# Kernel tuning notes

Measured on AMD Instinct MI355X. Metric: run time of the kernel, lower is better.

Reference implementation:

```python
import jax, jax.numpy as jnp
import numpy as np

B, L, D, H = 4, 2048, 512, 8
HD = D // H  # 64
MAX_REL = 4


def setup_inputs() -> dict:
    key = jax.random.key(0)
    ks = jax.random.split(key, 13)
    s = 1.0 / np.sqrt(D)
    return {
        "q": jax.random.normal(ks[0], (B, L, D), jnp.float32),
        "k": jax.random.normal(ks[1], (B, L, D), jnp.float32),
        "v": jax.random.normal(ks[2], (B, L, D), jnp.float32),
        "Wq": jax.random.normal(ks[3], (D, D), jnp.float32) * s,
        "bq": jax.random.normal(ks[4], (D,), jnp.float32) * 0.01,
        "Wk": jax.random.normal(ks[5], (D, D), jnp.float32) * s,
        "bk": jax.random.normal(ks[6], (D,), jnp.float32) * 0.01,
        "Wv": jax.random.normal(ks[7], (D, D), jnp.float32) * s,
        "bv": jax.random.normal(ks[8], (D,), jnp.float32) * 0.01,
        "Wo": jax.random.normal(ks[9], (D, D), jnp.float32) * s,
        "bo": jax.random.normal(ks[10], (D,), jnp.float32) * 0.01,
        "rel_k_table": jax.random.normal(ks[11], (2 * MAX_REL + 1, HD), jnp.float32),
        "rel_v_table": jax.random.normal(ks[12], (2 * MAX_REL + 1, HD), jnp.float32),
    }


def _to_heads(x):
    # [B, L, D] -> [B, H, L, HD]
    b, l, d = x.shape
    return x.reshape(b, l, H, d // H).transpose(0, 2, 1, 3)


def reference(q, k, v, Wq, bq, Wk, bk, Wv, bv, Wo, bo, rel_k_table, rel_v_table):
    # NOTE: in the source, the relative-attention output is overwritten by the
    # plain SDPA call immediately after, so observable math = SDPA only.
    # rel_k_table / rel_v_table are dead parameters (zero gradient).
    relu = jax.nn.relu
    qh = _to_heads(relu(q @ Wq.T + bq))  # [B,H,L,HD]
    kh = _to_heads(relu(k @ Wk.T + bk))
    vh = _to_heads(relu(v @ Wv.T + bv))
    # scale by sqrt(d_key)=sqrt(512), matching the original (not sqrt(head_dim))
    scores = jnp.einsum("bhqd,bhkd->bhqk", qh, kh) / jnp.sqrt(jnp.float32(D))
    attn = jax.nn.softmax(scores, axis=-1)
    out = jnp.einsum("bhqk,bhkd->bhqd", attn, vh)  # [B,H,L,HD]
    out = out.transpose(0, 2, 1, 3).reshape(B, L, D)
    return relu(out @ Wo.T + bo)
```

## Files before the change

### kernel.cpp

```cpp
#include <hip/hip_runtime.h>
#include <hip/hip_bf16.h>

#define B_  4
#define L_  2048
#define D_  512
#define H_  8
#define HD_ 64
#define M_  (B_ * L_)

typedef __bf16 bf16;
typedef __attribute__((ext_vector_type(8)))  __bf16 bf16x8;
typedef __attribute__((ext_vector_type(4)))  __bf16 bf16x4;
typedef __attribute__((ext_vector_type(16))) float  f32x16;

__device__ __forceinline__ f32x16 mfma32(bf16x8 a, bf16x8 b, f32x16 c) {
    return __builtin_amdgcn_mfma_f32_32x32x16_bf16(a, b, c, 0, 0, 0);
}

__device__ __forceinline__ void pack_body(const float* __restrict__ src,
                                          bf16* __restrict__ dst, int R,
                                          int m0, int k0)
{
    __shared__ __align__(16) bf16 tile[64][76];
    const int t = threadIdx.x;
#pragma unroll
    for (int rep = 0; rep < 4; rep++) {
        const int idx = rep * 256 + t;
        const int r = idx >> 4, c4 = idx & 15;
        const float4 f = *(const float4*)(src + (size_t)(m0 + r) * 512 + k0 + c4 * 4);
        bf16x4 v; v[0] = (bf16)f.x; v[1] = (bf16)f.y; v[2] = (bf16)f.z; v[3] = (bf16)f.w;
        *(bf16x4*)(&tile[r][c4 * 4]) = v;
    }
    __syncthreads();
#pragma unroll
    for (int rep = 0; rep < 2; rep++) {
        const int s = rep * 256 + t;
        const int ml = s & 63, kpl = s >> 6;
        const bf16x4 lo = *(const bf16x4*)(&tile[ml][kpl * 8]);
        const bf16x4 hi4 = *(const bf16x4*)(&tile[ml][kpl * 8 + 4]);
        bf16x8 v;
#pragma unroll
        for (int e = 0; e < 4; e++) { v[e] = lo[e]; v[e + 4] = hi4[e]; }
        *(bf16x8*)(dst + ((size_t)(k0 / 8 + kpl) * R + m0 + ml) * 8) = v;
    }
}

__global__ __launch_bounds__(256) void pack_all(
    const float* __restrict__ q, const float* __restrict__ k,
    const float* __restrict__ v,
    const float* __restrict__ W0, const float* __restrict__ W1,
    const float* __restrict__ W2, const float* __restrict__ W3,
    bf16* __restrict__ Wp, bf16* __restrict__ P0, bf16* __restrict__ P1,
    bf16* __restrict__ P2)
{
    const int z = blockIdx.z;
    if (z < 4) {
        if (blockIdx.x >= 8) return;
        const float* src = z == 0 ? W0 : z == 1 ? W1 : z == 2 ? W2 : W3;
        pack_body(src, Wp + (size_t)z * 64 * 512 * 8, 512, blockIdx.x * 64, blockIdx.y * 64);
    } else {
        const float* src = z == 4 ? q : z == 5 ? k : v;
        bf16* dst = z == 4 ? P0 : z == 5 ? P1 : P2;
        pack_body(src, dst, M_, blockIdx.x * 64, blockIdx.y * 64);
    }
}

struct PJob {
    const bf16* X; const bf16* W; const float* bias; void* out;
    float postmul; int mode;
};

__global__ __launch_bounds__(256, 3) void proj_kernel(PJob j0, PJob j1)
{
    const PJob jb = (blockIdx.z == 0) ? j0 : j1;
    const int w    = threadIdx.x >> 6;
    const int lane = threadIdx.x & 63;
    const int l31  = lane & 31;
    const int hi   = lane >> 5;
    const int m0 = blockIdx.x * 128;
    const int n0 = blockIdx.y * 64;
    const int mh = w & 1;
    const int nh = w >> 1;

    __shared__ __align__(16) bf16 Ab[2][16][64][8];
    __shared__ __align__(16) bf16 Bb[2][8][64][8];

    f32x16 acc[2];
#pragma unroll
    for (int mi = 0; mi < 2; mi++)
#pragma unroll
        for (int r = 0; r < 16; r++) acc[mi][r] = 0.0f;

    auto ldA = [&](int f, int k0) -> bf16x8 {
        return *(const bf16x8*)(jb.X + ((size_t)((k0 >> 3) + (f >> 2) * 2 + hi) * M_
                                        + m0 + (f & 3) * 32 + l31) * 8);
    };
    auto ldB = [&](int f, int k0) -> bf16x8 {
        return *(const bf16x8*)(jb.W + ((size_t)((k0 >> 3) + (f >> 1) * 2 + hi) * 512
                                        + n0 + (f & 1) * 32 + l31) * 8);
    };

    bf16x8 rA[3][4], rB[3][2];
#pragma unroll
    for (int i = 0; i < 4; i++) rA[0][i] = ldA(w * 4 + i, 0);
#pragma unroll
    for (int i = 0; i < 2; i++) rB[0][i] = ldB(w * 2 + i, 0);
#pragma unroll
    for (int i = 0; i < 4; i++) *(bf16x8*)(&Ab[0][w * 4 + i][lane][0]) = rA[0][i];
#pragma unroll
    for (int i = 0; i < 2; i++) *(bf16x8*)(&Bb[0][w * 2 + i][lane][0]) = rB[0][i];
#pragma unroll
    for (int s = 1; s < 3; s++) {
#pragma unroll
        for (int i = 0; i < 4; i++) rA[s][i] = ldA(w * 4 + i, s * 64);
#pragma unroll
        for (int i = 0; i < 2; i++) rB[s][i] = ldB(w * 2 + i, s * 64);
    }
    __syncthreads();

#pragma unroll
    for (int it = 0; it < 8; it++) {
        const int cur = it & 1;
        if (it < 5) {
            const int s = it % 3, kn = (it + 3) * 64;
#pragma unroll
            for (int i = 0; i < 4; i++) rA[s][i] = ldA(w * 4 + i, kn);
#pragma unroll
            for (int i = 0; i < 2; i++) rB[s][i] = ldB(w * 2 + i, kn);
        }
#pragma unroll
        for (int ks = 0; ks < 4; ks++) {
            const bf16x8 bfr = *(const bf16x8*)(&Bb[cur][ks * 2 + nh][lane][0]);
#pragma unroll
            for (int mi = 0; mi < 2; mi++) {
                const bf16x8 afr = *(const bf16x8*)(&Ab[cur][ks * 4 + mh * 2 + mi][lane][0]);
                acc[mi] = mfma32(afr, bfr, acc[mi]);
            }
        }
        if (it < 7) {
            const int s = (it + 1) % 3;
#pragma unroll
            for (int i = 0; i < 4; i++) *(bf16x8*)(&Ab[1 - cur][w * 4 + i][lane][0]) = rA[s][i];
#pragma unroll
            for (int i = 0; i < 2; i++) *(bf16x8*)(&Bb[1 - cur][w * 2 + i][lane][0]) = rB[s][i];
            __syncthreads();
        }
    }

    const int col = n0 + nh * 32 + l31;
    const float bn = jb.bias[col];
    const int mode = jb.mode;
#pragma unroll
    for (int mi = 0; mi < 2; mi++)
#pragma unroll
        for (int r = 0; r < 16; r++) {
            const int row = m0 + (mh * 2 + mi) * 32 + (r & 3) + 8 * (r >> 2) + 4 * hi;
            float v = fmaxf(acc[mi][r] + bn, 0.0f);
            if (mode == 2) {
                ((float*)jb.out)[(size_t)row * D_ + col] = v;
            } else {
                v *= jb.postmul;
                const int b = row >> 11, l = row & (L_ - 1);
                const int h = col >> 6,  hd = col & (HD_ - 1);
                const int bh = b * H_ + h;
                size_t idx;
                if (mode == 0) {
                    idx = ((size_t)bh * L_ + l) * HD_ + hd;
                } else if (mode == 1) {
                    idx = (((size_t)bh * 8 + (hd >> 3)) * L_ + l) * 8 + (hd & 7);
                } else {
                    const int swzl = (l & ~15) | (l & 3) | ((l & 4) << 1) | ((l & 8) >> 1);
                    idx = (((size_t)bh * 256 + (swzl >> 3)) * 64 + hd) * 8 + (swzl & 7);
                }
                ((bf16*)jb.out)[idx] = (bf16)v;
            }
        }
}

__global__ __launch_bounds__(128, 2) void attn_kernel(
    const bf16* __restrict__ qh, const bf16* __restrict__ Kp,
    const bf16* __restrict__ Vp, bf16* __restrict__ Op)
{
    const int w    = threadIdx.x >> 6;
    const int lane = threadIdx.x & 63;
    const int l31  = lane & 31;
    const int hi   = lane >> 5;
    const int bh   = blockIdx.y;
    const int qb   = blockIdx.x * 64 + w * 32;

    const bf16* Q   = qh + (size_t)bh * L_ * HD_;
    const bf16* Kpb = Kp + (size_t)bh * 8 * L_ * 8;
    const bf16* Vpb = Vp + (size_t)bh * 256 * 64 * 8;

    __shared__ __align__(16) bf16 Vb[2][8][64][8];

    bf16x8 qf[4];
#pragma unroll
    for (int ks = 0; ks < 4; ks++)
        qf[ks] = *(const bf16x8*)(Q + (size_t)(qb + l31) * HD_ + ks * 16 + hi * 8);

    f32x16 zz;
#pragma unroll
    for (int r = 0; r < 16; r++) zz[r] = 0.0f;
    f32x16 o0 = zz, o1 = zz, lacc = zz;
    bf16x8 ones;
#pragma unroll
    for (int u = 0; u < 8; u++) ones[u] = (bf16)1.0f;

    auto ldK = [&](int f, int t) -> bf16x8 {
        return *(const bf16x8*)(Kpb + ((size_t)((f >> 1) * 2 + hi) * L_
                                       + t * 64 + (f & 1) * 32 + l31) * 8);
    };
    auto ldV = [&](int f, int t) -> bf16x8 {
        return *(const bf16x8*)(Vpb + ((size_t)(t * 8 + (f >> 1) * 2 + hi) * 64
                                       + (f & 1) * 32 + l31) * 8);
    };

    bf16x8 kr[8], vr[2][4];
#pragma unroll
    for (int i = 0; i < 4; i++) vr[0][i] = ldV(w * 4 + i, 0);
#pragma unroll
    for (int i = 0; i < 4; i++) *(bf16x8*)(&Vb[0][w * 4 + i][lane][0]) = vr[0][i];
#pragma unroll
    for (int i = 0; i < 4; i++) vr[1][i] = ldV(w * 4 + i, 1);
#pragma unroll
    for (int i = 0; i < 4; i++) vr[0][i] = ldV(w * 4 + i, 2);
#pragma unroll
    for (int f = 0; f < 8; f++) kr[f] = ldK(f, 0);
    __syncthreads();

    auto tile_body = [&](int t, int cur, int nxt) {
        f32x16 s0 = mfma32(kr[0], qf[0], zz);
        f32x16 s1 = mfma32(kr[1], qf[0], zz);
#pragma unroll
        for (int ks = 1; ks < 4; ks++) {
            s0 = mfma32(kr[ks * 2 + 0], qf[ks], s0);
            s1 = mfma32(kr[ks * 2 + 1], qf[ks], s1);
        }
        if (t < 31) {
#pragma unroll
            for (int f = 0; f < 8; f++) kr[f] = ldK(f, t + 1);
        }

#pragma unroll
        for (int r = 0; r < 16; r++) s0[r] = __builtin_amdgcn_exp2f(s0[r]);
        {
            bf16x8 pf0, pf1;
#pragma unroll
            for (int u = 0; u < 8; u++) { pf0[u] = (bf16)s0[u]; pf1[u] = (bf16)s0[8 + u]; }
            o0   = mfma32(pf0, *(const bf16x8*)(&Vb[cur][0][lane][0]), o0);
            o1   = mfma32(pf0, *(const bf16x8*)(&Vb[cur][1][lane][0]), o1);
            lacc = mfma32(pf0, ones, lacc);
            o0   = mfma32(pf1, *(const bf16x8*)(&Vb[cur][2][lane][0]), o0);
            o1   = mfma32(pf1, *(const bf16x8*)(&Vb[cur][3][lane][0]), o1);
            lacc = mfma32(pf1, ones, lacc);
        }
#pragma unroll
        for (int r = 0; r < 16; r++) s1[r] = __builtin_amdgcn_exp2f(s1[r]);
        {
            bf16x8 pf2, pf3;
#pragma unroll
            for (int u = 0; u < 8; u++) { pf2[u] = (bf16)s1[u]; pf3[u] = (bf16)s1[8 + u]; }
            o0   = mfma32(pf2, *(const bf16x8*)(&Vb[cur][4][lane][0]), o0);
            o1   = mfma32(pf2, *(const bf16x8*)(&Vb[cur][5][lane][0]), o1);
            lacc = mfma32(pf2, ones, lacc);
            o0   = mfma32(pf3, *(const bf16x8*)(&Vb[cur][6][lane][0]), o0);
            o1   = mfma32(pf3, *(const bf16x8*)(&Vb[cur][7][lane][0]), o1);
            lacc = mfma32(pf3, ones, lacc);
        }

        if (t < 31) {
#pragma unroll
            for (int i = 0; i < 4; i++)
                *(bf16x8*)(&Vb[1 - cur][w * 4 + i][lane][0]) = vr[nxt][i];
            const int tn = (t + 3 < 32) ? t + 3 : 31;
#pragma unroll
            for (int i = 0; i < 4; i++) vr[nxt][i] = ldV(w * 4 + i, tn);
            __syncthreads();
        }
    };

    for (int tt = 0; tt < 16; tt++) {
        tile_body(2 * tt + 0, 0, 1);
        tile_body(2 * tt + 1, 1, 0);
    }

    const int b = bh >> 3, h = bh & 7;
#pragma unroll
    for (int r = 0; r < 16; r++) {
        const int rl = (r & 3) + 8 * (r >> 2) + 4 * hi;
        const float inv = 1.0f / lacc[r];
        const int m = b * L_ + qb + rl;
        const int c0 = h * HD_ + l31;
        Op[((size_t)(c0 >> 3) * M_ + m) * 8 + (c0 & 7)] = (bf16)(o0[r] * inv);
        const int c1 = c0 + 32;
        Op[((size_t)(c1 >> 3) * M_ + m) * 8 + (c1 & 7)] = (bf16)(o1[r] * inv);
    }
}

extern "C" void kernel_launch(void* const* d_in, const int* in_sizes, int n_in,
                              void* d_out, int out_size, void* d_ws, size_t ws_size,
                              hipStream_t stream)
{
    (void)in_sizes; (void)n_in; (void)out_size; (void)ws_size;
    const float* q  = (const float*)d_in[0];
    const float* k  = (const float*)d_in[1];
    const float* v  = (const float*)d_in[2];
    const float* Wq = (const float*)d_in[3];
    const float* bq = (const float*)d_in[4];
    const float* Wk = (const float*)d_in[5];
    const float* bk = (const float*)d_in[6];
    const float* Wv = (const float*)d_in[7];
    const float* bv = (const float*)d_in[8];
    const float* Wo = (const float*)d_in[9];
    const float* bo = (const float*)d_in[10];
    float* out = (float*)d_out;

    char* ws = (char*)d_ws;
    const size_t MB = 1024 * 1024;
    bf16* P0  = (bf16*)(ws);
    bf16* P1  = (bf16*)(ws + 8 * MB);
    bf16* P2  = (bf16*)(ws + 16 * MB);
    bf16* Wp  = (bf16*)(ws + 24 * MB);
    bf16* qh  = (bf16*)(d_out);
    bf16* Kp  = (bf16*)((char*)d_out + 8 * MB);
    bf16* Vp  = P0;
    bf16* Opb = P1;

    bf16* Wqp = Wp;
    bf16* Wkp = Wp + (size_t)64 * 512 * 8;
    bf16* Wvp = Wp + (size_t)2 * 64 * 512 * 8;
    bf16* Wop = Wp + (size_t)3 * 64 * 512 * 8;

    const float SCALE_LOG2E = 0.06377946282349575f;

    dim3 pb(256);
    pack_all<<<dim3(128, 8, 7), pb, 0, stream>>>(q, k, v, Wq, Wk, Wv, Wo,
                                                 Wp, P0, P1, P2);

    PJob jq{P0, Wqp, bq, qh, SCALE_LOG2E, 0};
    PJob jk{P1, Wkp, bk, Kp, 1.0f, 1};
    proj_kernel<<<dim3(64, 8, 2), pb, 0, stream>>>(jq, jk);

    PJob jv{P2, Wvp, bv, Vp, 1.0f, 3};
    proj_kernel<<<dim3(64, 8, 1), pb, 0, stream>>>(jv, jv);

    attn_kernel<<<dim3(32, 32), dim3(128), 0, stream>>>(qh, Kp, Vp, Opb);

    PJob jo{Opb, Wop, bo, out, 1.0f, 2};
    proj_kernel<<<dim3(64, 8, 1), pb, 0, stream>>>(jo, jo);
}
```

Before: 197.6 us.

## Use single-wave attention blocks with register V, XCD-aware mapping, fused QKV projection

The attention kernel moves from 2-wave blocks that share V through double-buffered LDS and barriers to 1-wave blocks that load V fragments straight into registers, so LDS and __syncthreads go away. Blocks are remapped so all query tiles of a given (batch, head) land on the same XCD, improving L2 reuse of K/V, and s_setprio is raised around the MFMA bursts. When the workspace is large enough, V gets its own buffer so the Q, K and V projections can run as one 3-way launch instead of two. The cost is more register pressure and duplicate global V loads per wave, relying on L2 hits to absorb them.

```diff
diff --git a/kernel.cpp b/kernel.cpp
--- a/kernel.cpp
+++ b/kernel.cpp
@@ -70,9 +70,9 @@
     float postmul; int mode;
 };
 
-__global__ __launch_bounds__(256, 3) void proj_kernel(PJob j0, PJob j1)
-{
-    const PJob jb = (blockIdx.z == 0) ? j0 : j1;
+__global__ __launch_bounds__(256, 3) void proj_kernel(PJob j0, PJob j1, PJob j2)
+{
+    const PJob jb = (blockIdx.z == 0) ? j0 : (blockIdx.z == 1) ? j1 : j2;
     const int w    = threadIdx.x >> 6;
     const int lane = threadIdx.x & 63;
     const int l31  = lane & 31;
@@ -177,22 +177,23 @@
         }
 }
 
-__global__ __launch_bounds__(128, 2) void attn_kernel(
+__global__ __launch_bounds__(64, 2) void attn_kernel(
     const bf16* __restrict__ qh, const bf16* __restrict__ Kp,
     const bf16* __restrict__ Vp, bf16* __restrict__ Op)
 {
-    const int w    = threadIdx.x >> 6;
-    const int lane = threadIdx.x & 63;
+    const int lane = threadIdx.x;
     const int l31  = lane & 31;
     const int hi   = lane >> 5;
-    const int bh   = blockIdx.y;
-    const int qb   = blockIdx.x * 64 + w * 32;
+
+    const int lin  = blockIdx.x + (blockIdx.y << 6);
+    const int xcd  = lin & 7;
+    const int slot = lin >> 3;
+    const int bh   = (xcd << 2) + (slot >> 6);
+    const int qb   = (slot & 63) << 5;
 
     const bf16* Q   = qh + (size_t)bh * L_ * HD_;
     const bf16* Kpb = Kp + (size_t)bh * 8 * L_ * 8;
     const bf16* Vpb = Vp + (size_t)bh * 256 * 64 * 8;
-
-    __shared__ __align__(16) bf16 Vb[2][8][64][8];
 
     bf16x8 qf[4];
 #pragma unroll
@@ -216,20 +217,15 @@
                                        + (f & 1) * 32 + l31) * 8);
     };
 
-    bf16x8 kr[8], vr[2][4];
-#pragma unroll
-    for (int i = 0; i < 4; i++) vr[0][i] = ldV(w * 4 + i, 0);
-#pragma unroll
-    for (int i = 0; i < 4; i++) *(bf16x8*)(&Vb[0][w * 4 + i][lane][0]) = vr[0][i];
-#pragma unroll
-    for (int i = 0; i < 4; i++) vr[1][i] = ldV(w * 4 + i, 1);
-#pragma unroll
-    for (int i = 0; i < 4; i++) vr[0][i] = ldV(w * 4 + i, 2);
+    bf16x8 kr[8], vf[8];
 #pragma unroll
     for (int f = 0; f < 8; f++) kr[f] = ldK(f, 0);
-    __syncthreads();
-
-    auto tile_body = [&](int t, int cur, int nxt) {
+#pragma unroll
+    for (int f = 0; f < 8; f++) vf[f] = ldV(f, 0);
+
+#pragma unroll 2
+    for (int t = 0; t < 32; t++) {
+        __builtin_amdgcn_s_setprio(1);
         f32x16 s0 = mfma32(kr[0], qf[0], zz);
         f32x16 s1 = mfma32(kr[1], qf[0], zz);
 #pragma unroll
@@ -237,6 +233,7 @@
             s0 = mfma32(kr[ks * 2 + 0], qf[ks], s0);
             s1 = mfma32(kr[ks * 2 + 1], qf[ks], s1);
         }
+        __builtin_amdgcn_s_setprio(0);
         if (t < 31) {
 #pragma unroll
             for (int f = 0; f < 8; f++) kr[f] = ldK(f, t + 1);
@@ -244,45 +241,39 @@
 
 #pragma unroll
         for (int r = 0; r < 16; r++) s0[r] = __builtin_amdgcn_exp2f(s0[r]);
-        {
-            bf16x8 pf0, pf1;
-#pragma unroll
-            for (int u = 0; u < 8; u++) { pf0[u] = (bf16)s0[u]; pf1[u] = (bf16)s0[8 + u]; }
-            o0   = mfma32(pf0, *(const bf16x8*)(&Vb[cur][0][lane][0]), o0);
-            o1   = mfma32(pf0, *(const bf16x8*)(&Vb[cur][1][lane][0]), o1);
-            lacc = mfma32(pf0, ones, lacc);
-            o0   = mfma32(pf1, *(const bf16x8*)(&Vb[cur][2][lane][0]), o0);
-            o1   = mfma32(pf1, *(const bf16x8*)(&Vb[cur][3][lane][0]), o1);
-            lacc = mfma32(pf1, ones, lacc);
-        }
+        bf16x8 pf0, pf1;
+#pragma unroll
+        for (int u = 0; u < 8; u++) { pf0[u] = (bf16)s0[u]; pf1[u] = (bf16)s0[8 + u]; }
+        __builtin_amdgcn_s_setprio(1);
+        o0   = mfma32(pf0, vf[0], o0);
+        o1   = mfma32(pf0, vf[1], o1);
+        lacc = mfma32(pf0, ones, lacc);
+        o0   = mfma32(pf1, vf[2], o0);
+        o1   = mfma32(pf1, vf[3], o1);
+        lacc = mfma32(pf1, ones, lacc);
+        __builtin_amdgcn_s_setprio(0);
+        if (t < 31) {
+#pragma unroll
+            for (int f = 0; f < 4; f++) vf[f] = ldV(f, t + 1);
+        }
+
 #pragma unroll
         for (int r = 0; r < 16; r++) s1[r] = __builtin_amdgcn_exp2f(s1[r]);
-        {
-            bf16x8 pf2, pf3;
-#pragma unroll
-            for (int u = 0; u < 8; u++) { pf2[u] = (bf16)s1[u]; pf3[u] = (bf16)s1[8 + u]; }
-            o0   = mfma32(pf2, *(const bf16x8*)(&Vb[cur][4][lane][0]), o0);
-            o1   = mfma32(pf2, *(const bf16x8*)(&Vb[cur][5][lane][0]), o1);
-            lacc = mfma32(pf2, ones, lacc);
-            o0   = mfma32(pf3, *(const bf16x8*)(&Vb[cur][6][lane][0]), o0);
-            o1   = mfma32(pf3, *(const bf16x8*)(&Vb[cur][7][lane][0]), o1);
-            lacc = mfma32(pf3, ones, lacc);
-        }
-
+        bf16x8 pf2, pf3;
+#pragma unroll
+        for (int u = 0; u < 8; u++) { pf2[u] = (bf16)s1[u]; pf3[u] = (bf16)s1[8 + u]; }
+        __builtin_amdgcn_s_setprio(1);
+        o0   = mfma32(pf2, vf[4], o0);
+        o1   = mfma32(pf2, vf[5], o1);
+        lacc = mfma32(pf2, ones, lacc);
+        o0   = mfma32(pf3, vf[6], o0);
+        o1   = mfma32(pf3, vf[7], o1);
+        lacc = mfma32(pf3, ones, lacc);
+        __builtin_amdgcn_s_setprio(0);
         if (t < 31) {
 #pragma unroll
-            for (int i = 0; i < 4; i++)
-                *(bf16x8*)(&Vb[1 - cur][w * 4 + i][lane][0]) = vr[nxt][i];
-            const int tn = (t + 3 < 32) ? t + 3 : 31;
-#pragma unroll
-            for (int i = 0; i < 4; i++) vr[nxt][i] = ldV(w * 4 + i, tn);
-            __syncthreads();
-        }
-    };
-
-    for (int tt = 0; tt < 16; tt++) {
-        tile_body(2 * tt + 0, 0, 1);
-        tile_body(2 * tt + 1, 1, 0);
+            for (int f = 4; f < 8; f++) vf[f] = ldV(f, t + 1);
+        }
     }
 
     const int b = bh >> 3, h = bh & 7;
@@ -302,7 +293,7 @@
                               void* d_out, int out_size, void* d_ws, size_t ws_size,
                               hipStream_t stream)
 {
-    (void)in_sizes; (void)n_in; (void)out_size; (void)ws_size;
+    (void)in_sizes; (void)n_in; (void)out_size;
     const float* q  = (const float*)d_in[0];
     const float* k  = (const float*)d_in[1];
     const float* v  = (const float*)d_in[2];
@@ -324,7 +315,6 @@
     bf16* Wp  = (bf16*)(ws + 24 * MB);
     bf16* qh  = (bf16*)(d_out);
     bf16* Kp  = (bf16*)((char*)d_out + 8 * MB);
-    bf16* Vp  = P0;
     bf16* Opb = P1;
 
     bf16* Wqp = Wp;
@@ -338,15 +328,26 @@
     pack_all<<<dim3(128, 8, 7), pb, 0, stream>>>(q, k, v, Wq, Wk, Wv, Wo,
                                                  Wp, P0, P1, P2);
 
-    PJob jq{P0, Wqp, bq, qh, SCALE_LOG2E, 0};
-    PJob jk{P1, Wkp, bk, Kp, 1.0f, 1};
-    proj_kernel<<<dim3(64, 8, 2), pb, 0, stream>>>(jq, jk);
-
-    PJob jv{P2, Wvp, bv, Vp, 1.0f, 3};
-    proj_kernel<<<dim3(64, 8, 1), pb, 0, stream>>>(jv, jv);
-
-    attn_kernel<<<dim3(32, 32), dim3(128), 0, stream>>>(qh, Kp, Vp, Opb);
+    if (ws_size >= (size_t)34 * MB) {
+        bf16* VpN = (bf16*)(ws + 26 * MB);
+        PJob jq{P0, Wqp, bq, qh,  SCALE_LOG2E, 0};
+        PJob jk{P1, Wkp, bk, Kp,  1.0f, 1};
+        PJob jv{P2, Wvp, bv, VpN, 1.0f, 3};
+        proj_kernel<<<dim3(64, 8, 3), pb, 0, stream>>>(jq, jk, jv);
+
+        attn_kernel<<<dim3(64, 32), dim3(64), 0, stream>>>(qh, Kp, VpN, Opb);
+    } else {
+        bf16* Vp = P0;
+        PJob jq{P0, Wqp, bq, qh, SCALE_LOG2E, 0};
+        PJob jk{P1, Wkp, bk, Kp, 1.0f, 1};
+        proj_kernel<<<dim3(64, 8, 2), pb, 0, stream>>>(jq, jk, jk);
+
+        PJob jv{P2, Wvp, bv, Vp, 1.0f, 3};
+        proj_kernel<<<dim3(64, 8, 1), pb, 0, stream>>>(jv, jv, jv);
+
+        attn_kernel<<<dim3(64, 32), dim3(64), 0, stream>>>(qh, Kp, Vp, Opb);
+    }
 
     PJob jo{Opb, Wop, bo, out, 1.0f, 2};
-    proj_kernel<<<dim3(64, 8, 1), pb, 0, stream>>>(jo, jo);
-}
+    proj_kernel<<<dim3(64, 8, 1), pb, 0, stream>>>(jo, jo, jo);
+}
```

After: 202.5 us. 2.5% more time.

## Fuse fp32-to-bf16 activation conversion into QKV projection and remap attention blocks per XCD

Applied to the files above, without the earlier changes.

The separate pack pass that converted q/k/v activations to bf16 is removed. The QKV projection now loads fp32 rows directly, converts them in registers before staging to shared memory, and runs Q, K and V in a single launch. Attention blocks are remapped so that each XCD handles a contiguous set of batch-heads, which is meant to improve L2 reuse of K/V. The cost is doubled global read bytes for A tiles and extra conversion work inside the GEMM loop, along with the register pressure that comes with it.

```diff
diff --git a/kernel.cpp b/kernel.cpp
--- a/kernel.cpp
+++ b/kernel.cpp
@@ -45,34 +45,24 @@
     }
 }
 
-__global__ __launch_bounds__(256) void pack_all(
-    const float* __restrict__ q, const float* __restrict__ k,
-    const float* __restrict__ v,
+__global__ __launch_bounds__(256) void pack_w(
     const float* __restrict__ W0, const float* __restrict__ W1,
     const float* __restrict__ W2, const float* __restrict__ W3,
-    bf16* __restrict__ Wp, bf16* __restrict__ P0, bf16* __restrict__ P1,
-    bf16* __restrict__ P2)
+    bf16* __restrict__ Wp)
 {
     const int z = blockIdx.z;
-    if (z < 4) {
-        if (blockIdx.x >= 8) return;
-        const float* src = z == 0 ? W0 : z == 1 ? W1 : z == 2 ? W2 : W3;
-        pack_body(src, Wp + (size_t)z * 64 * 512 * 8, 512, blockIdx.x * 64, blockIdx.y * 64);
-    } else {
-        const float* src = z == 4 ? q : z == 5 ? k : v;
-        bf16* dst = z == 4 ? P0 : z == 5 ? P1 : P2;
-        pack_body(src, dst, M_, blockIdx.x * 64, blockIdx.y * 64);
-    }
+    const float* src = z == 0 ? W0 : z == 1 ? W1 : z == 2 ? W2 : W3;
+    pack_body(src, Wp + (size_t)z * 64 * 512 * 8, 512, blockIdx.x * 64, blockIdx.y * 64);
 }
 
 struct PJob {
-    const bf16* X; const bf16* W; const float* bias; void* out;
-    float postmul; int mode;
+    const bf16* X; const float* Xf; const bf16* W; const float* bias;
+    void* out; float postmul; int mode;
 };
 
-__global__ __launch_bounds__(256, 3) void proj_kernel(PJob j0, PJob j1)
-{
-    const PJob jb = (blockIdx.z == 0) ? j0 : j1;
+template<bool FP32A>
+__device__ __forceinline__ void proj_body(const PJob jb)
+{
     const int w    = threadIdx.x >> 6;
     const int lane = threadIdx.x & 63;
     const int l31  = lane & 31;
@@ -95,38 +85,80 @@
         return *(const bf16x8*)(jb.X + ((size_t)((k0 >> 3) + (f >> 2) * 2 + hi) * M_
                                         + m0 + (f & 3) * 32 + l31) * 8);
     };
+    auto ldAf = [&](int f, int k0, float4* d) {
+        const int row  = m0 + (f & 3) * 32 + l31;
+        const int koct = (k0 >> 3) + (f >> 2) * 2 + hi;
+        const float* p = jb.Xf + (size_t)row * 512 + koct * 8;
+        d[0] = *(const float4*)p;
+        d[1] = *(const float4*)(p + 4);
+    };
+    auto cv8 = [](const float4* d) -> bf16x8 {
+        bf16x8 v;
+        v[0] = (bf16)d[0].x; v[1] = (bf16)d[0].y;
+        v[2] = (bf16)d[0].z; v[3] = (bf16)d[0].w;
+        v[4] = (bf16)d[1].x; v[5] = (bf16)d[1].y;
+        v[6] = (bf16)d[1].z; v[7] = (bf16)d[1].w;
+        return v;
+    };
     auto ldB = [&](int f, int k0) -> bf16x8 {
         return *(const bf16x8*)(jb.W + ((size_t)((k0 >> 3) + (f >> 1) * 2 + hi) * 512
                                         + n0 + (f & 1) * 32 + l31) * 8);
     };
 
-    bf16x8 rA[3][4], rB[3][2];
-#pragma unroll
-    for (int i = 0; i < 4; i++) rA[0][i] = ldA(w * 4 + i, 0);
+    bf16x8 rA[3][4];
+    float4 rAf[2][4][2];
+    bf16x8 rB[3][2];
+
+    if constexpr (FP32A) {
+#pragma unroll
+        for (int i = 0; i < 4; i++) ldAf(w * 4 + i, 0, rAf[0][i]);
+#pragma unroll
+        for (int i = 0; i < 4; i++)
+            *(bf16x8*)(&Ab[0][w * 4 + i][lane][0]) = cv8(rAf[0][i]);
+#pragma unroll
+        for (int i = 0; i < 4; i++) ldAf(w * 4 + i, 64, rAf[1][i]);
+    } else {
+#pragma unroll
+        for (int i = 0; i < 4; i++) rA[0][i] = ldA(w * 4 + i, 0);
+#pragma unroll
+        for (int i = 0; i < 4; i++)
+            *(bf16x8*)(&Ab[0][w * 4 + i][lane][0]) = rA[0][i];
+#pragma unroll
+        for (int s = 1; s < 3; s++)
+#pragma unroll
+            for (int i = 0; i < 4; i++) rA[s][i] = ldA(w * 4 + i, s * 64);
+    }
 #pragma unroll
     for (int i = 0; i < 2; i++) rB[0][i] = ldB(w * 2 + i, 0);
 #pragma unroll
-    for (int i = 0; i < 4; i++) *(bf16x8*)(&Ab[0][w * 4 + i][lane][0]) = rA[0][i];
-#pragma unroll
-    for (int i = 0; i < 2; i++) *(bf16x8*)(&Bb[0][w * 2 + i][lane][0]) = rB[0][i];
-#pragma unroll
-    for (int s = 1; s < 3; s++) {
-#pragma unroll
-        for (int i = 0; i < 4; i++) rA[s][i] = ldA(w * 4 + i, s * 64);
+    for (int i = 0; i < 2; i++)
+        *(bf16x8*)(&Bb[0][w * 2 + i][lane][0]) = rB[0][i];
+#pragma unroll
+    for (int s = 1; s < 3; s++)
 #pragma unroll
         for (int i = 0; i < 2; i++) rB[s][i] = ldB(w * 2 + i, s * 64);
-    }
     __syncthreads();
 
 #pragma unroll
     for (int it = 0; it < 8; it++) {
         const int cur = it & 1;
+        if constexpr (FP32A) {
+            if (it < 6) {
+#pragma unroll
+                for (int i = 0; i < 4; i++)
+                    ldAf(w * 4 + i, (it + 2) * 64, rAf[it & 1][i]);
+            }
+        } else {
+            if (it < 5) {
+#pragma unroll
+                for (int i = 0; i < 4; i++)
+                    rA[it % 3][i] = ldA(w * 4 + i, (it + 3) * 64);
+            }
+        }
         if (it < 5) {
-            const int s = it % 3, kn = (it + 3) * 64;
-#pragma unroll
-            for (int i = 0; i < 4; i++) rA[s][i] = ldA(w * 4 + i, kn);
-#pragma unroll
-            for (int i = 0; i < 2; i++) rB[s][i] = ldB(w * 2 + i, kn);
+#pragma unroll
+            for (int i = 0; i < 2; i++)
+                rB[it % 3][i] = ldB(w * 2 + i, (it + 3) * 64);
         }
 #pragma unroll
         for (int ks = 0; ks < 4; ks++) {
@@ -138,11 +170,18 @@
             }
         }
         if (it < 7) {
-            const int s = (it + 1) % 3;
-#pragma unroll
-            for (int i = 0; i < 4; i++) *(bf16x8*)(&Ab[1 - cur][w * 4 + i][lane][0]) = rA[s][i];
-#pragma unroll
-            for (int i = 0; i < 2; i++) *(bf16x8*)(&Bb[1 - cur][w * 2 + i][lane][0]) = rB[s][i];
+            if constexpr (FP32A) {
+#pragma unroll
+                for (int i = 0; i < 4; i++)
+                    *(bf16x8*)(&Ab[1 - cur][w * 4 + i][lane][0]) = cv8(rAf[(it + 1) & 1][i]);
+            } else {
+#pragma unroll
+                for (int i = 0; i < 4; i++)
+                    *(bf16x8*)(&Ab[1 - cur][w * 4 + i][lane][0]) = rA[(it + 1) % 3][i];
+            }
+#pragma unroll
+            for (int i = 0; i < 2; i++)
+                *(bf16x8*)(&Bb[1 - cur][w * 2 + i][lane][0]) = rB[(it + 1) % 3][i];
             __syncthreads();
         }
     }
@@ -177,6 +216,18 @@
         }
 }
 
+__global__ __launch_bounds__(256, 3) void proj_kernel(PJob j0, PJob j1, PJob j2)
+{
+    const PJob jb = (blockIdx.z == 0) ? j0 : (blockIdx.z == 1) ? j1 : j2;
+    proj_body<false>(jb);
+}
+
+__global__ __launch_bounds__(256, 3) void proj_qkv_kernel(PJob j0, PJob j1, PJob j2)
+{
+    const PJob jb = (blockIdx.z == 0) ? j0 : (blockIdx.z == 1) ? j1 : j2;
+    proj_body<true>(jb);
+}
+
 __global__ __launch_bounds__(128, 2) void attn_kernel(
     const bf16* __restrict__ qh, const bf16* __restrict__ Kp,
     const bf16* __restrict__ Vp, bf16* __restrict__ Op)
@@ -185,8 +236,12 @@
     const int lane = threadIdx.x & 63;
     const int l31  = lane & 31;
     const int hi   = lane >> 5;
-    const int bh   = blockIdx.y;
-    const int qb   = blockIdx.x * 64 + w * 32;
+
+    const int lin  = blockIdx.x + (blockIdx.y << 5);
+    const int xcd  = lin & 7;
+    const int slot = lin >> 3;
+    const int bh   = (xcd << 2) + (slot >> 5);
+    const int qb   = (slot & 31) * 64 + w * 32;
 
     const bf16* Q   = qh + (size_t)bh * L_ * HD_;
     const bf16* Kpb = Kp + (size_t)bh * 8 * L_ * 8;
@@ -318,14 +373,11 @@
 
     char* ws = (char*)d_ws;
     const size_t MB = 1024 * 1024;
-    bf16* P0  = (bf16*)(ws);
-    bf16* P1  = (bf16*)(ws + 8 * MB);
-    bf16* P2  = (bf16*)(ws + 16 * MB);
-    bf16* Wp  = (bf16*)(ws + 24 * MB);
+    bf16* Vp  = (bf16*)(ws);
+    bf16* Opb = (bf16*)(ws + 8 * MB);
+    bf16* Wp  = (bf16*)(ws + 16 * MB);
     bf16* qh  = (bf16*)(d_out);
     bf16* Kp  = (bf16*)((char*)d_out + 8 * MB);
-    bf16* Vp  = P0;
-    bf16* Opb = P1;
 
     bf16* Wqp = Wp;
     bf16* Wkp = Wp + (size_t)64 * 512 * 8;
@@ -334,19 +386,15 @@
 
     const float SCALE_LOG2E = 0.06377946282349575f;
 
-    dim3 pb(256);
-    pack_all<<<dim3(128, 8, 7), pb, 0, stream>>>(q, k, v, Wq, Wk, Wv, Wo,
-                                                 Wp, P0, P1, P2);
-
-    PJob jq{P0, Wqp, bq, qh, SCALE_LOG2E, 0};
-    PJob jk{P1, Wkp, bk, Kp, 1.0f, 1};
-    proj_kernel<<<dim3(64, 8, 2), pb, 0, stream>>>(jq, jk);
-
-    PJob jv{P2, Wvp, bv, Vp, 1.0f, 3};
-    proj_kernel<<<dim3(64, 8, 1), pb, 0, stream>>>(jv, jv);
+    pack_w<<<dim3(8, 8, 4), dim3(256), 0, stream>>>(Wq, Wk, Wv, Wo, Wp);
+
+    PJob jq{nullptr, q, Wqp, bq, qh, SCALE_LOG2E, 0};
+    PJob jk{nullptr, k, Wkp, bk, Kp, 1.0f, 1};
+    PJob jv{nullptr, v, Wvp, bv, Vp, 1.0f, 3};
+    proj_qkv_kernel<<<dim3(64, 8, 3), dim3(256), 0, stream>>>(jq, jk, jv);
 
     attn_kernel<<<dim3(32, 32), dim3(128), 0, stream>>>(qh, Kp, Vp, Opb);
 
-    PJob jo{Opb, Wop, bo, out, 1.0f, 2};
-    proj_kernel<<<dim3(64, 8, 1), pb, 0, stream>>>(jo, jo);
-}
+    PJob jo{Opb, nullptr, Wop, bo, out, 1.0f, 2};
+    proj_kernel<<<dim3(64, 8, 1), dim3(256), 0, stream>>>(jo, jo, jo);
+}
```

Result: slower. 217.8 us (+10.2%).

## Widen projection tile to 128x128, fuse Q/K/V projections, remap attention blocks per XCD

Applied to the files above, without the earlier changes.

The projection GEMM tile grows from 128x64 to 128x128, with each wave computing a 2x2 set of MFMA accumulators. The prefetch pipeline drops from three register stages to two. When the workspace is large enough, the Q, K and V projections run in a single launch by writing V to a separate workspace buffer, which removes a kernel launch and its serialization. Attention blocks are remapped so that all query blocks of a head land on the same XCD, aiming for better L2 reuse of K/V. In exchange, register pressure rises and occupancy is lower (launch bounds go from 3 to 2 blocks).

```diff
diff --git a/kernel.cpp b/kernel.cpp
--- a/kernel.cpp
+++ b/kernel.cpp
@@ -70,111 +70,115 @@
     float postmul; int mode;
 };
 
-__global__ __launch_bounds__(256, 3) void proj_kernel(PJob j0, PJob j1)
-{
-    const PJob jb = (blockIdx.z == 0) ? j0 : j1;
+__global__ __launch_bounds__(256, 2) void proj_kernel(PJob j0, PJob j1, PJob j2)
+{
+    const PJob jb = (blockIdx.z == 0) ? j0 : (blockIdx.z == 1) ? j1 : j2;
     const int w    = threadIdx.x >> 6;
     const int lane = threadIdx.x & 63;
     const int l31  = lane & 31;
     const int hi   = lane >> 5;
     const int m0 = blockIdx.x * 128;
-    const int n0 = blockIdx.y * 64;
+    const int n0 = blockIdx.y * 128;
     const int mh = w & 1;
     const int nh = w >> 1;
 
     __shared__ __align__(16) bf16 Ab[2][16][64][8];
-    __shared__ __align__(16) bf16 Bb[2][8][64][8];
-
-    f32x16 acc[2];
+    __shared__ __align__(16) bf16 Bb[2][16][64][8];
+
+    f32x16 acc[2][2];
 #pragma unroll
     for (int mi = 0; mi < 2; mi++)
 #pragma unroll
-        for (int r = 0; r < 16; r++) acc[mi][r] = 0.0f;
+        for (int ni = 0; ni < 2; ni++)
+#pragma unroll
+            for (int r = 0; r < 16; r++) acc[mi][ni][r] = 0.0f;
 
     auto ldA = [&](int f, int k0) -> bf16x8 {
         return *(const bf16x8*)(jb.X + ((size_t)((k0 >> 3) + (f >> 2) * 2 + hi) * M_
                                         + m0 + (f & 3) * 32 + l31) * 8);
     };
     auto ldB = [&](int f, int k0) -> bf16x8 {
-        return *(const bf16x8*)(jb.W + ((size_t)((k0 >> 3) + (f >> 1) * 2 + hi) * 512
-                                        + n0 + (f & 1) * 32 + l31) * 8);
-    };
-
-    bf16x8 rA[3][4], rB[3][2];
-#pragma unroll
-    for (int i = 0; i < 4; i++) rA[0][i] = ldA(w * 4 + i, 0);
-#pragma unroll
-    for (int i = 0; i < 2; i++) rB[0][i] = ldB(w * 2 + i, 0);
-#pragma unroll
-    for (int i = 0; i < 4; i++) *(bf16x8*)(&Ab[0][w * 4 + i][lane][0]) = rA[0][i];
-#pragma unroll
-    for (int i = 0; i < 2; i++) *(bf16x8*)(&Bb[0][w * 2 + i][lane][0]) = rB[0][i];
-#pragma unroll
-    for (int s = 1; s < 3; s++) {
-#pragma unroll
-        for (int i = 0; i < 4; i++) rA[s][i] = ldA(w * 4 + i, s * 64);
-#pragma unroll
-        for (int i = 0; i < 2; i++) rB[s][i] = ldB(w * 2 + i, s * 64);
-    }
+        return *(const bf16x8*)(jb.W + ((size_t)((k0 >> 3) + (f >> 2) * 2 + hi) * 512
+                                        + n0 + (f & 3) * 32 + l31) * 8);
+    };
+
+    bf16x8 rA[2][4], rB[2][4];
+#pragma unroll
+    for (int i = 0; i < 4; i++) { rA[0][i] = ldA(w * 4 + i, 0);  rB[0][i] = ldB(w * 4 + i, 0); }
+#pragma unroll
+    for (int i = 0; i < 4; i++) {
+        *(bf16x8*)(&Ab[0][w * 4 + i][lane][0]) = rA[0][i];
+        *(bf16x8*)(&Bb[0][w * 4 + i][lane][0]) = rB[0][i];
+    }
+#pragma unroll
+    for (int i = 0; i < 4; i++) { rA[1][i] = ldA(w * 4 + i, 64);  rB[1][i] = ldB(w * 4 + i, 64); }
+#pragma unroll
+    for (int i = 0; i < 4; i++) { rA[0][i] = ldA(w * 4 + i, 128); rB[0][i] = ldB(w * 4 + i, 128); }
     __syncthreads();
 
 #pragma unroll
     for (int it = 0; it < 8; it++) {
         const int cur = it & 1;
-        if (it < 5) {
-            const int s = it % 3, kn = (it + 3) * 64;
-#pragma unroll
-            for (int i = 0; i < 4; i++) rA[s][i] = ldA(w * 4 + i, kn);
-#pragma unroll
-            for (int i = 0; i < 2; i++) rB[s][i] = ldB(w * 2 + i, kn);
-        }
 #pragma unroll
         for (int ks = 0; ks < 4; ks++) {
-            const bf16x8 bfr = *(const bf16x8*)(&Bb[cur][ks * 2 + nh][lane][0]);
-#pragma unroll
-            for (int mi = 0; mi < 2; mi++) {
-                const bf16x8 afr = *(const bf16x8*)(&Ab[cur][ks * 4 + mh * 2 + mi][lane][0]);
-                acc[mi] = mfma32(afr, bfr, acc[mi]);
+            const bf16x8 a0 = *(const bf16x8*)(&Ab[cur][ks * 4 + mh * 2 + 0][lane][0]);
+            const bf16x8 a1 = *(const bf16x8*)(&Ab[cur][ks * 4 + mh * 2 + 1][lane][0]);
+            const bf16x8 b0 = *(const bf16x8*)(&Bb[cur][ks * 4 + nh * 2 + 0][lane][0]);
+            const bf16x8 b1 = *(const bf16x8*)(&Bb[cur][ks * 4 + nh * 2 + 1][lane][0]);
+            acc[0][0] = mfma32(a0, b0, acc[0][0]);
+            acc[0][1] = mfma32(a0, b1, acc[0][1]);
+            acc[1][0] = mfma32(a1, b0, acc[1][0]);
+            acc[1][1] = mfma32(a1, b1, acc[1][1]);
+        }
+        if (it < 7) {
+            const int s = (it + 1) & 1;
+#pragma unroll
+            for (int i = 0; i < 4; i++) {
+                *(bf16x8*)(&Ab[1 - cur][w * 4 + i][lane][0]) = rA[s][i];
+                *(bf16x8*)(&Bb[1 - cur][w * 4 + i][lane][0]) = rB[s][i];
             }
-        }
-        if (it < 7) {
-            const int s = (it + 1) % 3;
-#pragma unroll
-            for (int i = 0; i < 4; i++) *(bf16x8*)(&Ab[1 - cur][w * 4 + i][lane][0]) = rA[s][i];
-#pragma unroll
-            for (int i = 0; i < 2; i++) *(bf16x8*)(&Bb[1 - cur][w * 2 + i][lane][0]) = rB[s][i];
+            if (it < 5) {
+#pragma unroll
+                for (int i = 0; i < 4; i++) {
+                    rA[s][i] = ldA(w * 4 + i, (it + 3) * 64);
+                    rB[s][i] = ldB(w * 4 + i, (it + 3) * 64);
+                }
+            }
             __syncthreads();
         }
     }
 
-    const int col = n0 + nh * 32 + l31;
-    const float bn = jb.bias[col];
     const int mode = jb.mode;
 #pragma unroll
-    for (int mi = 0; mi < 2; mi++)
-#pragma unroll
-        for (int r = 0; r < 16; r++) {
-            const int row = m0 + (mh * 2 + mi) * 32 + (r & 3) + 8 * (r >> 2) + 4 * hi;
-            float v = fmaxf(acc[mi][r] + bn, 0.0f);
-            if (mode == 2) {
-                ((float*)jb.out)[(size_t)row * D_ + col] = v;
-            } else {
-                v *= jb.postmul;
-                const int b = row >> 11, l = row & (L_ - 1);
-                const int h = col >> 6,  hd = col & (HD_ - 1);
-                const int bh = b * H_ + h;
-                size_t idx;
-                if (mode == 0) {
-                    idx = ((size_t)bh * L_ + l) * HD_ + hd;
-                } else if (mode == 1) {
-                    idx = (((size_t)bh * 8 + (hd >> 3)) * L_ + l) * 8 + (hd & 7);
+    for (int ni = 0; ni < 2; ni++) {
+        const int col = n0 + (nh * 2 + ni) * 32 + l31;
+        const float bn = jb.bias[col];
+#pragma unroll
+        for (int mi = 0; mi < 2; mi++)
+#pragma unroll
+            for (int r = 0; r < 16; r++) {
+                const int row = m0 + (mh * 2 + mi) * 32 + (r & 3) + 8 * (r >> 2) + 4 * hi;
+                float v = fmaxf(acc[mi][ni][r] + bn, 0.0f);
+                if (mode == 2) {
+                    ((float*)jb.out)[(size_t)row * D_ + col] = v;
                 } else {
-                    const int swzl = (l & ~15) | (l & 3) | ((l & 4) << 1) | ((l & 8) >> 1);
-                    idx = (((size_t)bh * 256 + (swzl >> 3)) * 64 + hd) * 8 + (swzl & 7);
+                    v *= jb.postmul;
+                    const int b = row >> 11, l = row & (L_ - 1);
+                    const int h = col >> 6,  hd = col & (HD_ - 1);
+                    const int bh = b * H_ + h;
+                    size_t idx;
+                    if (mode == 0) {
+                        idx = ((size_t)bh * L_ + l) * HD_ + hd;
+                    } else if (mode == 1) {
+                        idx = (((size_t)bh * 8 + (hd >> 3)) * L_ + l) * 8 + (hd & 7);
+                    } else {
+                        const int swzl = (l & ~15) | (l & 3) | ((l & 4) << 1) | ((l & 8) >> 1);
+                        idx = (((size_t)bh * 256 + (swzl >> 3)) * 64 + hd) * 8 + (swzl & 7);
+                    }
+                    ((bf16*)jb.out)[idx] = (bf16)v;
                 }
-                ((bf16*)jb.out)[idx] = (bf16)v;
             }
-        }
+    }
 }
 
 __global__ __launch_bounds__(128, 2) void attn_kernel(
@@ -185,8 +189,12 @@
     const int lane = threadIdx.x & 63;
     const int l31  = lane & 31;
     const int hi   = lane >> 5;
-    const int bh   = blockIdx.y;
-    const int qb   = blockIdx.x * 64 + w * 32;
+
+    const int lin  = blockIdx.x + (blockIdx.y << 5);
+    const int xcd  = lin & 7;
+    const int slot = lin >> 3;
+    const int bh   = (xcd << 2) + (slot >> 5);
+    const int qb   = (slot & 31) * 64 + w * 32;
 
     const bf16* Q   = qh + (size_t)bh * L_ * HD_;
     const bf16* Kpb = Kp + (size_t)bh * 8 * L_ * 8;
@@ -302,7 +310,7 @@
                               void* d_out, int out_size, void* d_ws, size_t ws_size,
                               hipStream_t stream)
 {
-    (void)in_sizes; (void)n_in; (void)out_size; (void)ws_size;
+    (void)in_sizes; (void)n_in; (void)out_size;
     const float* q  = (const float*)d_in[0];
     const float* k  = (const float*)d_in[1];
     const float* v  = (const float*)d_in[2];
@@ -324,7 +332,6 @@
     bf16* Wp  = (bf16*)(ws + 24 * MB);
     bf16* qh  = (bf16*)(d_out);
     bf16* Kp  = (bf16*)((char*)d_out + 8 * MB);
-    bf16* Vp  = P0;
     bf16* Opb = P1;
 
     bf16* Wqp = Wp;
@@ -338,15 +345,26 @@
     pack_all<<<dim3(128, 8, 7), pb, 0, stream>>>(q, k, v, Wq, Wk, Wv, Wo,
                                                  Wp, P0, P1, P2);
 
-    PJob jq{P0, Wqp, bq, qh, SCALE_LOG2E, 0};
-    PJob jk{P1, Wkp, bk, Kp, 1.0f, 1};
-    proj_kernel<<<dim3(64, 8, 2), pb, 0, stream>>>(jq, jk);
-
-    PJob jv{P2, Wvp, bv, Vp, 1.0f, 3};
-    proj_kernel<<<dim3(64, 8, 1), pb, 0, stream>>>(jv, jv);
-
-    attn_kernel<<<dim3(32, 32), dim3(128), 0, stream>>>(qh, Kp, Vp, Opb);
+    if (ws_size >= (size_t)34 * MB) {
+        bf16* VpN = (bf16*)(ws + 26 * MB);
+        PJob jq{P0, Wqp, bq, qh,  SCALE_LOG2E, 0};
+        PJob jk{P1, Wkp, bk, Kp,  1.0f, 1};
+        PJob jv{P2, Wvp, bv, VpN, 1.0f, 3};
+        proj_kernel<<<dim3(64, 4, 3), pb, 0, stream>>>(jq, jk, jv);
+
+        attn_kernel<<<dim3(32, 32), dim3(128), 0, stream>>>(qh, Kp, VpN, Opb);
+    } else {
+        bf16* Vp = P0;
+        PJob jq{P0, Wqp, bq, qh, SCALE_LOG2E, 0};
+        PJob jk{P1, Wkp, bk, Kp, 1.0f, 1};
+        proj_kernel<<<dim3(64, 4, 2), pb, 0, stream>>>(jq, jk, jk);
+
+        PJob jv{P2, Wvp, bv, Vp, 1.0f, 3};
+        proj_kernel<<<dim3(64, 4, 1), pb, 0, stream>>>(jv, jv, jv);
+
+        attn_kernel<<<dim3(32, 32), dim3(128), 0, stream>>>(qh, Kp, Vp, Opb);
+    }
 
     PJob jo{Opb, Wop, bo, out, 1.0f, 2};
-    proj_kernel<<<dim3(64, 8, 1), pb, 0, stream>>>(jo, jo);
-}
+    proj_kernel<<<dim3(64, 4, 1), pb, 0, stream>>>(jo, jo, jo);
+}
```

New measurement: 201.7 us. 1.02x slower.
